# Performance work log

Hardware: AMD Instinct MI355X
Metric: run time of the kernel (lower is better)

The kernel has to match this reference:

```python
import jax, jax.numpy as jnp
import numpy as np

I, T, L, E, H, W, V = 256, 256, 25, 128, 7, 7, 10000


def setup_inputs() -> dict:
    key = jax.random.key(0)
    k1, k2, k3, k4 = jax.random.split(key, 4)
    image_features = jax.random.normal(k1, (I, E, H, W), jnp.float32)
    text = jax.random.randint(k2, (T, L), 1, V)  # token ids (0 is padding idx)
    text_length = jax.random.randint(k3, (T,), 1, L + 1)  # lengths >= 1
    embedding = jax.random.normal(k4, (V, E), jnp.float32) * 0.02
    embedding = embedding.at[0].set(0.0)  # padding_idx=0 -> zero vector
    logit_scale = jnp.asarray(np.log(1.0 / 0.07), jnp.float32)
    return {
        'image_features': image_features,
        'embedding': embedding,
        'logit_scale': logit_scale,
        'text': text,
        'text_length': text_length,
    }


def reference(image_features, embedding, logit_scale, text, text_length):
    # text encoder: plain embedding lookup -> [T, L, E]
    text_features = embedding[text]
    # sim == 'max': per-word max over the 7x7 image patches
    # [I, T, L, H, W] intermediate (the kernel-fusion target)
    sims = jnp.einsum('iehw,tle->itlhw', image_features, text_features)
    match_max = jnp.max(sims, axis=(3, 4))  # [I, T, L]
    match_avg = jnp.sum(match_max, axis=2) / text_length.astype(jnp.float32)  # [I, T]
    scale = jnp.exp(logit_scale)
    logits_per_image = match_avg * scale          # [I, T]
    logits_per_text = match_avg.T * scale         # [T, I]
    return logits_per_image, logits_per_text
```

## Files before the change

kernel.cpp:

```cpp
#include <hip/hip_runtime.h>
#include <hip/hip_bf16.h>
#include <stdint.h>

#define NI 256
#define NT 256
#define NL 25
#define NE 128
#define NHW 49
#define NTL (NT*NL)

#define WAVES 8
#define CH_T 16
#define CH_TILES 25

typedef __attribute__((ext_vector_type(4))) int i32x4;

__device__ __forceinline__ int pack4(int q0, int q1, int q2, int q3) {
    return (q0 & 255) | ((q1 & 255) << 8) | ((q2 & 255) << 16) | ((q3 & 255) << 24);
}

__global__ __launch_bounds__(256) void prep_kernel(
    const float* __restrict__ emb, const int* __restrict__ text,
    const float* __restrict__ img,
    char* __restrict__ tf3, char* __restrict__ P2, char* __restrict__ P48,
    float* __restrict__ tfs, float* __restrict__ pscale)
{
    __shared__ float tile[NE * NHW];
    __shared__ float red[256];
    const int bid = blockIdx.x;
    const int tid = threadIdx.x;

    if (bid < 400) {
        int r   = tid >> 4;
        int sub = tid & 15;
        int row = bid * 16 + r;
        int tok = text[row];
        const float4* e4 = reinterpret_cast<const float4*>(emb + (size_t)tok * NE + sub * 8);
        float4 f0 = e4[0], f1 = e4[1];
        float m = fmaxf(fmaxf(fmaxf(fabsf(f0.x), fabsf(f0.y)), fmaxf(fabsf(f0.z), fabsf(f0.w))),
                        fmaxf(fmaxf(fabsf(f1.x), fabsf(f1.y)), fmaxf(fabsf(f1.z), fabsf(f1.w))));
        m = fmaxf(m, __shfl_xor(m, 1));
        m = fmaxf(m, __shfl_xor(m, 2));
        m = fmaxf(m, __shfl_xor(m, 4));
        m = fmaxf(m, __shfl_xor(m, 8));
        float s = (m > 0.f) ? 127.f / m : 0.f;
        if (sub == 0) tfs[row] = m / 127.f;
        int q0 = __float2int_rn(f0.x * s), q1 = __float2int_rn(f0.y * s);
        int q2 = __float2int_rn(f0.z * s), q3 = __float2int_rn(f0.w * s);
        int q4 = __float2int_rn(f1.x * s), q5 = __float2int_rn(f1.y * s);
        int q6 = __float2int_rn(f1.z * s), q7 = __float2int_rn(f1.w * s);
        int2 o = make_int2(pack4(q0, q1, q2, q3), pack4(q4, q5, q6, q7));
        int kh  = sub >> 3;
        int lhi = (sub >> 1) & 3;
        size_t addr = ((size_t)(bid * 2 + kh) * 64 + lhi * 16 + r) * 16 + (sub & 1) * 8;
        *reinterpret_cast<int2*>(tf3 + addr) = o;
    } else {
        int i = bid - 400;
        const float4* src4 = reinterpret_cast<const float4*>(img + (size_t)i * NE * NHW);
        float4* tile4 = reinterpret_cast<float4*>(tile);
        for (int idx = tid; idx < NE * NHW / 4; idx += 256) tile4[idx] = src4[idx];
        __syncthreads();
        float lm = 0.f;
        for (int idx = tid; idx < NE * NHW; idx += 256) lm = fmaxf(lm, fabsf(tile[idx]));
        red[tid] = lm;
        __syncthreads();
        #pragma unroll
        for (int st = 128; st > 0; st >>= 1) {
            if (tid < st) red[tid] = fmaxf(red[tid], red[tid + st]);
            __syncthreads();
        }
        float pmax = red[0];
        float s = (pmax > 0.f) ? 127.f / pmax : 0.f;
        if (tid == 0) pscale[i] = pmax / 127.f;

        for (int idx = tid; idx < 384; idx += 256) {
            int f = idx >> 6, lane = idx & 63;
            int mt = f >> 1, kh = f & 1;
            int lr = lane & 15, lhi = lane >> 4;
            int p = mt * 16 + lr;
            int d[4];
            #pragma unroll
            for (int w = 0; w < 4; w++) {
                int e = kh * 64 + lhi * 16 + w * 4;
                d[w] = pack4(__float2int_rn(tile[(e + 0) * NHW + p] * s),
                             __float2int_rn(tile[(e + 1) * NHW + p] * s),
                             __float2int_rn(tile[(e + 2) * NHW + p] * s),
                             __float2int_rn(tile[(e + 3) * NHW + p] * s));
            }
            i32x4 o = { d[0], d[1], d[2], d[3] };
            *reinterpret_cast<i32x4*>(P2 + ((size_t)(i * 6 + f) * 64 + lane) * 16) = o;
        }
        if (tid < 8) {
            int kh = tid & 1, lhi = (tid >> 1) & 3;
            int g = i >> 3, lr0 = i & 7;
            int d[4];
            #pragma unroll
            for (int w = 0; w < 4; w++) {
                int e = kh * 64 + lhi * 16 + w * 4;
                d[w] = pack4(__float2int_rn(tile[(e + 0) * NHW + 48] * s),
                             __float2int_rn(tile[(e + 1) * NHW + 48] * s),
                             __float2int_rn(tile[(e + 2) * NHW + 48] * s),
                             __float2int_rn(tile[(e + 3) * NHW + 48] * s));
            }
            i32x4 o = { d[0], d[1], d[2], d[3] };
            *reinterpret_cast<i32x4*>(P48 + ((size_t)(g * 2 + kh) * 64 + lhi * 16 + lr0) * 16) = o;
        }
    }
}

__global__ __launch_bounds__(512, 4) void match_kernel(
    const char* __restrict__ tf3,
    const char* __restrict__ P2,
    const char* __restrict__ P48,
    const float* __restrict__ tfs,
    const float* __restrict__ pscale,
    const int* __restrict__ text_length,
    const float* __restrict__ logit_scale,
    float* __restrict__ out)
{
    __shared__ int vals[WAVES][CH_TILES][64];
    __shared__ int vals48[CH_TILES][128];

    const int ig   = blockIdx.x & 31;
    const int tq   = blockIdx.x >> 5;
    const int tid  = threadIdx.x;
    const int wave = tid >> 6;
    const int lane = tid & 63;
    const int lr   = lane & 15;
    const int lhi  = lane >> 4;

    const int img = ig * WAVES + wave;
    const i32x4* p2 = reinterpret_cast<const i32x4*>(P2) + (size_t)img * 6 * 64 + lane;
    i32x4 pf[6];
    #pragma unroll
    for (int f = 0; f < 6; f++) pf[f] = p2[f * 64];
    #pragma unroll
    for (int f = 0; f < 6; f++) asm volatile("" : "+v"(pf[f]));

    const i32x4* p48 = reinterpret_cast<const i32x4*>(P48) + (size_t)ig * 2 * 64 + lane;

    i32x4 zc = { 0, 0, 0, 0 };
    asm volatile("" : "+v"(zc));

    const char* tb = tf3 + (size_t)tq * CH_TILES * 2048 + lane * 16;

    auto loadT = [&](i32x4* T, int jl) {
        T[0] = *reinterpret_cast<const i32x4*>(tb + jl * 2048);
        T[1] = *reinterpret_cast<const i32x4*>(tb + jl * 2048 + 1024);
    };

    auto imax = [](int a, int b) { return a > b ? a : b; };

    auto compute = [&](const i32x4* T, int jl) {
        __builtin_amdgcn_s_setprio(1);
        i32x4 a0 = __builtin_amdgcn_mfma_i32_16x16x64_i8(pf[0], T[0], zc, 0, 0, 0);
        i32x4 a1 = __builtin_amdgcn_mfma_i32_16x16x64_i8(pf[2], T[0], zc, 0, 0, 0);
        i32x4 a2 = __builtin_amdgcn_mfma_i32_16x16x64_i8(pf[4], T[0], zc, 0, 0, 0);
        a0 = __builtin_amdgcn_mfma_i32_16x16x64_i8(pf[1], T[1], a0, 0, 0, 0);
        a1 = __builtin_amdgcn_mfma_i32_16x16x64_i8(pf[3], T[1], a1, 0, 0, 0);
        a2 = __builtin_amdgcn_mfma_i32_16x16x64_i8(pf[5], T[1], a2, 0, 0, 0);
        if ((jl & 7) == wave) {
            i32x4 d = __builtin_amdgcn_mfma_i32_16x16x64_i8(p48[0],  T[0], zc, 0, 0, 0);
            d = __builtin_amdgcn_mfma_i32_16x16x64_i8(p48[64], T[1], d, 0, 0, 0);
            __builtin_amdgcn_s_setprio(0);
            if (lhi < 2) {
                #pragma unroll
                for (int r = 0; r < 4; r++)
                    vals48[jl][(lhi * 4 + r) * 16 + lr] = d[r];
            }
        } else {
            __builtin_amdgcn_s_setprio(0);
        }
        int r1 = imax(imax(a0[0], a0[1]), a0[2]);
        int r2 = imax(imax(a0[3], a1[0]), a1[1]);
        int r3 = imax(imax(a1[2], a1[3]), a2[0]);
        int r4 = imax(imax(a2[1], a2[2]), a2[3]);
        vals[wave][jl][lane] = imax(imax(r1, r2), imax(r3, r4));
    };

    i32x4 A[2], B[2];
    loadT(A, 0);
    #pragma unroll 1
    for (int jj = 0; jj < 12; jj++) {
        loadT(B, 2 * jj + 1);
        compute(A, 2 * jj);
        loadT(A, 2 * jj + 2);
        compute(B, 2 * jj + 1);
    }
    compute(A, 24);
    __syncthreads();

    if (tid < WAVES * CH_T) {
        int g  = tid >> 4;
        int tl = tid & 15;
        float simg = pscale[ig * WAVES + g];
        const float* tf_s = tfs + tq * 400;
        float s = 0.f;
        #pragma unroll
        for (int l = 0; l < 25; l++) {
            int row = tl * 25 + l;
            int j = row >> 4;
            int r = row & 15;
            int m0 = imax(vals[g][j][r],      vals[g][j][r + 16]);
            int m1 = imax(vals[g][j][r + 32], vals[g][j][r + 48]);
            int mm = imax(imax(m0, m1), vals48[j][g * 16 + r]);
            s += (float)mm * tf_s[row];
        }
        int t = tq * CH_T + tl;
        int i = ig * WAVES + g;
        float val = s * simg / (float)text_length[t] * expf(logit_scale[0]);
        out[(size_t)i * NT + t] = val;
        out[(size_t)NI * NT + (size_t)t * NI + i] = val;
    }
}

extern "C" void kernel_launch(void* const* d_in, const int* in_sizes, int n_in,
                              void* d_out, int out_size, void* d_ws, size_t ws_size,
                              hipStream_t stream)
{
    const float* img  = (const float*)d_in[0];
    const float* emb  = (const float*)d_in[1];
    const float* ls   = (const float*)d_in[2];
    const int*   text = (const int*)d_in[3];
    const int*   tlen = (const int*)d_in[4];
    float* out = (float*)d_out;

    char* ws = (char*)d_ws;
    char*  tf3    = ws;
    char*  P2     = ws + 819200;
    char*  P48    = ws + 2392064;
    float* tfs    = (float*)(ws + 2457600);
    float* pscale = (float*)(ws + 2483200);

    prep_kernel<<<656, 256, 0, stream>>>(emb, text, img, tf3, P2, P48, tfs, pscale);
    match_kernel<<<512, 512, 0, stream>>>(tf3, P2, P48, tfs, pscale, tlen, ls, out);
}
```

Measured before the change: 23.12 us.

## Split text tiles across wave pairs, shrink LDS scratch, fuse image absmax

The match kernel now gives each image to two waves that handle alternating text tiles. Blocks cover 4 images instead of 8, so the grid doubles to 1024 blocks and occupancy is raised to 8. Per-tile maxima are kept in LDS as shorts after an arithmetic shift by 7, and the 128 factor is put back through pscale. This halves the LDS footprint but drops low bits of the integer dot products, so results are slightly less exact. The prep kernel also computes the image absmax while loading the tile and reduces it with wave shuffles, removing the shared-memory tree reduction and most of its barriers.

```diff
diff --git a/kernel.cpp b/kernel.cpp
--- a/kernel.cpp
+++ b/kernel.cpp
@@ -7,9 +7,7 @@
 #define NL 25
 #define NE 128
 #define NHW 49
-#define NTL (NT*NL)
-
-#define WAVES 8
+
 #define CH_T 16
 #define CH_TILES 25
 
@@ -26,7 +24,7 @@
     float* __restrict__ tfs, float* __restrict__ pscale)
 {
     __shared__ float tile[NE * NHW];
-    __shared__ float red[256];
+    __shared__ float red[4];
     const int bid = blockIdx.x;
     const int tid = threadIdx.x;
 
@@ -58,18 +56,18 @@
         int i = bid - 400;
         const float4* src4 = reinterpret_cast<const float4*>(img + (size_t)i * NE * NHW);
         float4* tile4 = reinterpret_cast<float4*>(tile);
-        for (int idx = tid; idx < NE * NHW / 4; idx += 256) tile4[idx] = src4[idx];
+        float lm = 0.f;
+        for (int idx = tid; idx < NE * NHW / 4; idx += 256) {
+            float4 v = src4[idx];
+            tile4[idx] = v;
+            lm = fmaxf(lm, fmaxf(fmaxf(fabsf(v.x), fabsf(v.y)),
+                                 fmaxf(fabsf(v.z), fabsf(v.w))));
+        }
+        #pragma unroll
+        for (int d = 1; d < 64; d <<= 1) lm = fmaxf(lm, __shfl_xor(lm, d));
+        if ((tid & 63) == 0) red[tid >> 6] = lm;
         __syncthreads();
-        float lm = 0.f;
-        for (int idx = tid; idx < NE * NHW; idx += 256) lm = fmaxf(lm, fabsf(tile[idx]));
-        red[tid] = lm;
-        __syncthreads();
-        #pragma unroll
-        for (int st = 128; st > 0; st >>= 1) {
-            if (tid < st) red[tid] = fmaxf(red[tid], red[tid + st]);
-            __syncthreads();
-        }
-        float pmax = red[0];
+        float pmax = fmaxf(fmaxf(red[0], red[1]), fmaxf(red[2], red[3]));
         float s = (pmax > 0.f) ? 127.f / pmax : 0.f;
         if (tid == 0) pscale[i] = pmax / 127.f;
 
@@ -92,7 +90,7 @@
         }
         if (tid < 8) {
             int kh = tid & 1, lhi = (tid >> 1) & 3;
-            int g = i >> 3, lr0 = i & 7;
+            int g4 = i >> 2, r0 = i & 3;
             int d[4];
             #pragma unroll
             for (int w = 0; w < 4; w++) {
@@ -103,33 +101,31 @@
                              __float2int_rn(tile[(e + 3) * NHW + 48] * s));
             }
             i32x4 o = { d[0], d[1], d[2], d[3] };
-            *reinterpret_cast<i32x4*>(P48 + ((size_t)(g * 2 + kh) * 64 + lhi * 16 + lr0) * 16) = o;
-        }
-    }
-}
-
-__global__ __launch_bounds__(512, 4) void match_kernel(
-    const char* __restrict__ tf3,
-    const char* __restrict__ P2,
-    const char* __restrict__ P48,
-    const float* __restrict__ tfs,
-    const float* __restrict__ pscale,
-    const int* __restrict__ text_length,
-    const float* __restrict__ logit_scale,
-    float* __restrict__ out)
+            *reinterpret_cast<i32x4*>(P48 + ((size_t)(g4 * 2 + kh) * 64 + lhi * 16 + r0) * 16) = o;
+        }
+    }
+}
+
+__global__ __launch_bounds__(512, 8) void match_kernel(
+    const char* __restrict__ tf3, const char* __restrict__ P2,
+    const char* __restrict__ P48, const float* __restrict__ tfs,
+    const float* __restrict__ pscale, const int* __restrict__ text_length,
+    const float* __restrict__ logit_scale, float* __restrict__ out)
 {
-    __shared__ int vals[WAVES][CH_TILES][64];
-    __shared__ int vals48[CH_TILES][128];
-
-    const int ig   = blockIdx.x & 31;
-    const int tq   = blockIdx.x >> 5;
+    __shared__ short vals[4][CH_TILES][64];
+    __shared__ short vals48[CH_TILES][64];
+
+    const int ig   = blockIdx.x & 63;
+    const int tq   = blockIdx.x >> 6;
     const int tid  = threadIdx.x;
     const int wave = tid >> 6;
+    const int il   = wave >> 1;
+    const int half = wave & 1;
     const int lane = tid & 63;
     const int lr   = lane & 15;
     const int lhi  = lane >> 4;
 
-    const int img = ig * WAVES + wave;
+    const int img = ig * 4 + il;
     const i32x4* p2 = reinterpret_cast<const i32x4*>(P2) + (size_t)img * 6 * 64 + lane;
     i32x4 pf[6];
     #pragma unroll
@@ -163,10 +159,10 @@
             i32x4 d = __builtin_amdgcn_mfma_i32_16x16x64_i8(p48[0],  T[0], zc, 0, 0, 0);
             d = __builtin_amdgcn_mfma_i32_16x16x64_i8(p48[64], T[1], d, 0, 0, 0);
             __builtin_amdgcn_s_setprio(0);
-            if (lhi < 2) {
+            if (lhi == 0) {
                 #pragma unroll
                 for (int r = 0; r < 4; r++)
-                    vals48[jl][(lhi * 4 + r) * 16 + lr] = d[r];
+                    vals48[jl][r * 16 + lr] = (short)(d[r] >> 7);
             }
         } else {
             __builtin_amdgcn_s_setprio(0);
@@ -175,39 +171,52 @@
         int r2 = imax(imax(a0[3], a1[0]), a1[1]);
         int r3 = imax(imax(a1[2], a1[3]), a2[0]);
         int r4 = imax(imax(a2[1], a2[2]), a2[3]);
-        vals[wave][jl][lane] = imax(imax(r1, r2), imax(r3, r4));
+        int v = imax(imax(r1, r2), imax(r3, r4));
+        vals[il][jl][lane] = (short)(v >> 7);
     };
 
     i32x4 A[2], B[2];
-    loadT(A, 0);
+    loadT(A, half);
+    int j = half;
     #pragma unroll 1
-    for (int jj = 0; jj < 12; jj++) {
-        loadT(B, 2 * jj + 1);
-        compute(A, 2 * jj);
-        loadT(A, 2 * jj + 2);
-        compute(B, 2 * jj + 1);
-    }
-    compute(A, 24);
+    for (int jj = 0; jj < 5; jj++) {
+        loadT(B, j + 2);
+        compute(A, j);
+        loadT(A, j + 4);
+        compute(B, j + 2);
+        j += 4;
+    }
+    if (half == 0) {
+        loadT(B, 22);
+        compute(A, 20);
+        loadT(A, 24);
+        compute(B, 22);
+        compute(A, 24);
+    } else {
+        loadT(B, 23);
+        compute(A, 21);
+        compute(B, 23);
+    }
     __syncthreads();
 
-    if (tid < WAVES * CH_T) {
+    if (tid < 4 * CH_T) {
         int g  = tid >> 4;
         int tl = tid & 15;
-        float simg = pscale[ig * WAVES + g];
+        float simg = pscale[ig * 4 + g] * 128.f;
         const float* tf_s = tfs + tq * 400;
         float s = 0.f;
         #pragma unroll
         for (int l = 0; l < 25; l++) {
             int row = tl * 25 + l;
-            int j = row >> 4;
-            int r = row & 15;
-            int m0 = imax(vals[g][j][r],      vals[g][j][r + 16]);
-            int m1 = imax(vals[g][j][r + 32], vals[g][j][r + 48]);
-            int mm = imax(imax(m0, m1), vals48[j][g * 16 + r]);
+            int jt = row >> 4;
+            int r  = row & 15;
+            int m0 = imax((int)vals[g][jt][r],      (int)vals[g][jt][r + 16]);
+            int m1 = imax((int)vals[g][jt][r + 32], (int)vals[g][jt][r + 48]);
+            int mm = imax(imax(m0, m1), (int)vals48[jt][g * 16 + r]);
             s += (float)mm * tf_s[row];
         }
         int t = tq * CH_T + tl;
-        int i = ig * WAVES + g;
+        int i = ig * 4 + g;
         float val = s * simg / (float)text_length[t] * expf(logit_scale[0]);
         out[(size_t)i * NT + t] = val;
         out[(size_t)NI * NT + (size_t)t * NI + i] = val;
@@ -229,9 +238,9 @@
     char*  tf3    = ws;
     char*  P2     = ws + 819200;
     char*  P48    = ws + 2392064;
-    float* tfs    = (float*)(ws + 2457600);
-    float* pscale = (float*)(ws + 2483200);
+    float* tfs    = (float*)(ws + 2523136);
+    float* pscale = (float*)(ws + 2548736);
 
     prep_kernel<<<656, 256, 0, stream>>>(emb, text, img, tf3, P2, P48, tfs, pscale);
-    match_kernel<<<512, 512, 0, stream>>>(tf3, P2, P48, tfs, pscale, tlen, ls, out);
-}
+    match_kernel<<<1024, 512, 0, stream>>>(tf3, P2, P48, tfs, pscale, tlen, ls, out);
+}
```

Result: slower. 39.81 us (+72.2%).

## Halve text chunk per block, double grid, store per-tile maxima as shorts in LDS

Applied to the files above, without the earlier changes.

Each block now covers 8 texts (200 rows, 13 tiles of 16 with overlap) instead of 16, and the grid doubles to 1024 blocks so more work runs concurrently. Per-tile max values are shifted right by 7 and kept as shorts, which halves LDS use and raises occupancy, and a factor of 128 is folded back into the scale. Because adjacent chunks overlap, some tiles are recomputed, and the truncating shift loses low-order precision in the int8 dot products.

```diff
diff --git a/kernel.cpp b/kernel.cpp
--- a/kernel.cpp
+++ b/kernel.cpp
@@ -7,11 +7,10 @@
 #define NL 25
 #define NE 128
 #define NHW 49
-#define NTL (NT*NL)
 
 #define WAVES 8
-#define CH_T 16
-#define CH_TILES 25
+#define CH_T 8
+#define NTIL 13
 
 typedef __attribute__((ext_vector_type(4))) int i32x4;
 
@@ -109,17 +108,13 @@
 }
 
 __global__ __launch_bounds__(512, 4) void match_kernel(
-    const char* __restrict__ tf3,
-    const char* __restrict__ P2,
-    const char* __restrict__ P48,
-    const float* __restrict__ tfs,
-    const float* __restrict__ pscale,
-    const int* __restrict__ text_length,
-    const float* __restrict__ logit_scale,
-    float* __restrict__ out)
+    const char* __restrict__ tf3, const char* __restrict__ P2,
+    const char* __restrict__ P48, const float* __restrict__ tfs,
+    const float* __restrict__ pscale, const int* __restrict__ text_length,
+    const float* __restrict__ logit_scale, float* __restrict__ out)
 {
-    __shared__ int vals[WAVES][CH_TILES][64];
-    __shared__ int vals48[CH_TILES][128];
+    __shared__ short vals[WAVES][NTIL][64];
+    __shared__ short vals48[NTIL][128];
 
     const int ig   = blockIdx.x & 31;
     const int tq   = blockIdx.x >> 5;
@@ -129,6 +124,8 @@
     const int lr   = lane & 15;
     const int lhi  = lane >> 4;
 
+    const int jg0 = (tq * 200) >> 4;
+
     const int img = ig * WAVES + wave;
     const i32x4* p2 = reinterpret_cast<const i32x4*>(P2) + (size_t)img * 6 * 64 + lane;
     i32x4 pf[6];
@@ -142,7 +139,7 @@
     i32x4 zc = { 0, 0, 0, 0 };
     asm volatile("" : "+v"(zc));
 
-    const char* tb = tf3 + (size_t)tq * CH_TILES * 2048 + lane * 16;
+    const char* tb = tf3 + (size_t)jg0 * 2048 + lane * 16;
 
     auto loadT = [&](i32x4* T, int jl) {
         T[0] = *reinterpret_cast<const i32x4*>(tb + jl * 2048);
@@ -166,7 +163,7 @@
             if (lhi < 2) {
                 #pragma unroll
                 for (int r = 0; r < 4; r++)
-                    vals48[jl][(lhi * 4 + r) * 16 + lr] = d[r];
+                    vals48[jl][(lhi * 4 + r) * 16 + lr] = (short)(d[r] >> 7);
             }
         } else {
             __builtin_amdgcn_s_setprio(0);
@@ -175,38 +172,37 @@
         int r2 = imax(imax(a0[3], a1[0]), a1[1]);
         int r3 = imax(imax(a1[2], a1[3]), a2[0]);
         int r4 = imax(imax(a2[1], a2[2]), a2[3]);
-        vals[wave][jl][lane] = imax(imax(r1, r2), imax(r3, r4));
+        vals[wave][jl][lane] = (short)(imax(imax(r1, r2), imax(r3, r4)) >> 7);
     };
 
     i32x4 A[2], B[2];
     loadT(A, 0);
     #pragma unroll 1
-    for (int jj = 0; jj < 12; jj++) {
+    for (int jj = 0; jj < 6; jj++) {
         loadT(B, 2 * jj + 1);
         compute(A, 2 * jj);
         loadT(A, 2 * jj + 2);
         compute(B, 2 * jj + 1);
     }
-    compute(A, 24);
+    compute(A, 12);
     __syncthreads();
 
     if (tid < WAVES * CH_T) {
-        int g  = tid >> 4;
-        int tl = tid & 15;
-        float simg = pscale[ig * WAVES + g];
-        const float* tf_s = tfs + tq * 400;
+        int g  = tid >> 3;
+        int tl = tid & 7;
+        int t  = tq * CH_T + tl;
+        float simg = pscale[ig * WAVES + g] * 128.f;
         float s = 0.f;
         #pragma unroll
         for (int l = 0; l < 25; l++) {
-            int row = tl * 25 + l;
-            int j = row >> 4;
-            int r = row & 15;
-            int m0 = imax(vals[g][j][r],      vals[g][j][r + 16]);
-            int m1 = imax(vals[g][j][r + 32], vals[g][j][r + 48]);
-            int mm = imax(imax(m0, m1), vals48[j][g * 16 + r]);
-            s += (float)mm * tf_s[row];
-        }
-        int t = tq * CH_T + tl;
+            int row = t * 25 + l;
+            int jt  = (row >> 4) - jg0;
+            int r   = row & 15;
+            int m0 = imax((int)vals[g][jt][r],      (int)vals[g][jt][r + 16]);
+            int m1 = imax((int)vals[g][jt][r + 32], (int)vals[g][jt][r + 48]);
+            int mm = imax(imax(m0, m1), (int)vals48[jt][g * 16 + r]);
+            s += (float)mm * tfs[row];
+        }
         int i = ig * WAVES + g;
         float val = s * simg / (float)text_length[t] * expf(logit_scale[0]);
         out[(size_t)i * NT + t] = val;
@@ -233,5 +229,5 @@
     float* pscale = (float*)(ws + 2483200);
 
     prep_kernel<<<656, 256, 0, stream>>>(emb, text, img, tf3, P2, P48, tfs, pscale);
-    match_kernel<<<512, 512, 0, stream>>>(tf3, P2, P48, tfs, pscale, tlen, ls, out);
-}
+    match_kernel<<<1024, 512, 0, stream>>>(tf3, P2, P48, tfs, pscale, tlen, ls, out);
+}
```

Result: slower. 24.30 us (+5.1%).
